# Kernel optimization log

Hardware: AMD Instinct MI355X
Metric: run time of the kernel (lower is better)

The kernel has to match this reference:

```python
import jax, jax.numpy as jnp
import numpy as np

ENT = 500000
REL = 1000
D = 128
N = 65536


def setup_inputs() -> dict:
    key = jax.random.key(0)
    ks = jax.random.split(key, 9)
    pos_h = jax.random.randint(ks[0], (N,), 0, ENT)
    pos_t = jax.random.randint(ks[1], (N,), 0, ENT)
    pos_r = jax.random.randint(ks[2], (N,), 0, REL)
    neg_h = jax.random.randint(ks[3], (N,), 0, ENT)
    neg_t = jax.random.randint(ks[4], (N,), 0, ENT)
    neg_r = jax.random.randint(ks[5], (N,), 0, REL)
    # entity embeddings: xavier-init then L2-row-normalized
    ent = jax.random.normal(ks[6], (ENT, D), dtype=jnp.float32)
    ent = ent / jnp.linalg.norm(ent, axis=1, keepdims=True)
    # vvrel embeddings: plain randn (sized entity_total in the original)
    vvrel = jax.random.normal(ks[7], (ENT, D), dtype=jnp.float32)
    # relation bases: L2-row-normalized
    bases = jax.random.normal(ks[8], (REL, D), dtype=jnp.float32)
    bases = bases / jnp.linalg.norm(bases, axis=1, keepdims=True)
    return {"pos_h": pos_h, "pos_t": pos_t, "pos_r": pos_r,
            "neg_h": neg_h, "neg_t": neg_t, "neg_r": neg_r,
            "ent_emb": ent, "vvrel_emb": vvrel, "bases": bases}


def _hyperplane_project(x, v):
    # (I - v v^T / (v.v)) x, applied row-wise without materializing [N,d,d]
    coef = jnp.sum(v * x, axis=-1, keepdims=True) / jnp.sum(v * v, axis=-1, keepdims=True)
    return x - coef * v


def reference(pos_h, pos_t, pos_r, neg_h, neg_t, neg_r, ent_emb, vvrel_emb, bases):
    v_pos = bases[pos_r]  # [N, D]; original uses pos_r projection for BOTH pos and neg
    ph = _hyperplane_project(ent_emb[pos_h], v_pos)
    pt = _hyperplane_project(ent_emb[pos_t], v_pos)
    pr = _hyperplane_project(vvrel_emb[pos_r], v_pos)
    nh = _hyperplane_project(ent_emb[neg_h], v_pos)
    nt = _hyperplane_project(ent_emb[neg_t], v_pos)
    nr = _hyperplane_project(vvrel_emb[neg_r], v_pos)
    # L1_flag = True
    pos = jnp.sum(jnp.abs(ph + pr - pt), axis=1)
    neg = jnp.sum(jnp.abs(nh + nr - nt), axis=1)
    return (pos, neg)
```

## Files before the change

### kernel.cpp

```cpp
#include <hip/hip_runtime.h>

#define NSAMP 65536
#define DDIM  128

__global__ __launch_bounds__(256) void transh_kernel(
    const int* __restrict__ pos_h, const int* __restrict__ pos_t, const int* __restrict__ pos_r,
    const int* __restrict__ neg_h, const int* __restrict__ neg_t, const int* __restrict__ neg_r,
    const float* __restrict__ ent, const float* __restrict__ vvrel, const float* __restrict__ bases,
    float* __restrict__ out)
{
    const int tid  = blockIdx.x * blockDim.x + threadIdx.x;
    const int samp = tid >> 5;
    const int sub  = threadIdx.x & 31;
    if (samp >= NSAMP) return;

    const int ph_i = pos_h[samp];
    const int pt_i = pos_t[samp];
    const int pr_i = pos_r[samp];
    const int nh_i = neg_h[samp];
    const int nt_i = neg_t[samp];
    const int nr_i = neg_r[samp];

    const float4* v4   = (const float4*)(bases + (size_t)pr_i * DDIM);
    const float4* ph4  = (const float4*)(ent   + (size_t)ph_i * DDIM);
    const float4* pt4  = (const float4*)(ent   + (size_t)pt_i * DDIM);
    const float4* prv4 = (const float4*)(vvrel + (size_t)pr_i * DDIM);
    const float4* nh4  = (const float4*)(ent   + (size_t)nh_i * DDIM);
    const float4* nt4  = (const float4*)(ent   + (size_t)nt_i * DDIM);
    const float4* nrv4 = (const float4*)(vvrel + (size_t)nr_i * DDIM);

    const float4 v  = v4[sub];
    const float4 a  = ph4[sub];
    const float4 c  = pt4[sub];
    const float4 b  = prv4[sub];
    const float4 na = nh4[sub];
    const float4 nc = nt4[sub];
    const float4 nb = nrv4[sub];

    float4 sp, sn;
    sp.x = a.x + b.x - c.x;  sp.y = a.y + b.y - c.y;
    sp.z = a.z + b.z - c.z;  sp.w = a.w + b.w - c.w;
    sn.x = na.x + nb.x - nc.x;  sn.y = na.y + nb.y - nc.y;
    sn.z = na.z + nb.z - nc.z;  sn.w = na.w + nb.w - nc.w;

    float vv  = v.x * v.x + v.y * v.y + v.z * v.z + v.w * v.w;
    float vsp = v.x * sp.x + v.y * sp.y + v.z * sp.z + v.w * sp.w;
    float vsn = v.x * sn.x + v.y * sn.y + v.z * sn.z + v.w * sn.w;

    #pragma unroll
    for (int off = 16; off > 0; off >>= 1) {
        vv  += __shfl_xor(vv,  off, 64);
        vsp += __shfl_xor(vsp, off, 64);
        vsn += __shfl_xor(vsn, off, 64);
    }

    const float cp = vsp / vv;
    const float cn = vsn / vv;

    float ap = fabsf(sp.x - cp * v.x) + fabsf(sp.y - cp * v.y)
             + fabsf(sp.z - cp * v.z) + fabsf(sp.w - cp * v.w);
    float an = fabsf(sn.x - cn * v.x) + fabsf(sn.y - cn * v.y)
             + fabsf(sn.z - cn * v.z) + fabsf(sn.w - cn * v.w);

    #pragma unroll
    for (int off = 16; off > 0; off >>= 1) {
        ap += __shfl_xor(ap, off, 64);
        an += __shfl_xor(an, off, 64);
    }

    if (sub == 0) {
        out[samp]         = ap;
        out[NSAMP + samp] = an;
    }
}

extern "C" void kernel_launch(void* const* d_in, const int* in_sizes, int n_in,
                              void* d_out, int out_size, void* d_ws, size_t ws_size,
                              hipStream_t stream) {
    const int*   pos_h = (const int*)d_in[0];
    const int*   pos_t = (const int*)d_in[1];
    const int*   pos_r = (const int*)d_in[2];
    const int*   neg_h = (const int*)d_in[3];
    const int*   neg_t = (const int*)d_in[4];
    const int*   neg_r = (const int*)d_in[5];
    const float* ent   = (const float*)d_in[6];
    const float* vvrel = (const float*)d_in[7];
    const float* bases = (const float*)d_in[8];
    float* out = (float*)d_out;

    const int threads = 256;
    const int blocks  = (NSAMP * 32) / threads;
    transh_kernel<<<blocks, threads, 0, stream>>>(
        pos_h, pos_t, pos_r, neg_h, neg_t, neg_r, ent, vvrel, bases, out);
}
```

Baseline: 419.4 us.

## Process four samples per half-wave with double-buffered row gathers

Each 32-lane group now handles four consecutive samples instead of one. All indices are loaded up front, and the seven gathered embedding rows for the next sample are prefetched into a second register buffer while the current sample is reduced. The goal is to keep more gather loads in flight per wave and to hide memory latency behind the shuffle reductions. In exchange the grid is four times smaller and register use rises, which may lower occupancy. The bounds check was also dropped, which is safe only because NSAMP divides evenly.

```diff
diff --git a/kernel.cpp b/kernel.cpp
--- a/kernel.cpp
+++ b/kernel.cpp
@@ -2,6 +2,7 @@
 
 #define NSAMP 65536
 #define DDIM  128
+#define SPT   4
 
 __global__ __launch_bounds__(256) void transh_kernel(
     const int* __restrict__ pos_h, const int* __restrict__ pos_t, const int* __restrict__ pos_r,
@@ -10,67 +11,84 @@
     float* __restrict__ out)
 {
     const int tid  = blockIdx.x * blockDim.x + threadIdx.x;
-    const int samp = tid >> 5;
+    const int hw   = tid >> 5;
     const int sub  = threadIdx.x & 31;
-    if (samp >= NSAMP) return;
+    const int base = hw * SPT;
 
-    const int ph_i = pos_h[samp];
-    const int pt_i = pos_t[samp];
-    const int pr_i = pos_r[samp];
-    const int nh_i = neg_h[samp];
-    const int nt_i = neg_t[samp];
-    const int nr_i = neg_r[samp];
+    int iph[SPT], ipt[SPT], ipr[SPT], inh[SPT], itn[SPT], inr[SPT];
+    #pragma unroll
+    for (int k = 0; k < SPT; ++k) {
+        const int s = base + k;
+        iph[k] = pos_h[s];  ipt[k] = pos_t[s];  ipr[k] = pos_r[s];
+        inh[k] = neg_h[s];  itn[k] = neg_t[s];  inr[k] = neg_r[s];
+    }
 
-    const float4* v4   = (const float4*)(bases + (size_t)pr_i * DDIM);
-    const float4* ph4  = (const float4*)(ent   + (size_t)ph_i * DDIM);
-    const float4* pt4  = (const float4*)(ent   + (size_t)pt_i * DDIM);
-    const float4* prv4 = (const float4*)(vvrel + (size_t)pr_i * DDIM);
-    const float4* nh4  = (const float4*)(ent   + (size_t)nh_i * DDIM);
-    const float4* nt4  = (const float4*)(ent   + (size_t)nt_i * DDIM);
-    const float4* nrv4 = (const float4*)(vvrel + (size_t)nr_i * DDIM);
+    float4 V[2], A[2], B[2], C[2], NA[2], NB[2], NC[2];
 
-    const float4 v  = v4[sub];
-    const float4 a  = ph4[sub];
-    const float4 c  = pt4[sub];
-    const float4 b  = prv4[sub];
-    const float4 na = nh4[sub];
-    const float4 nc = nt4[sub];
-    const float4 nb = nrv4[sub];
-
-    float4 sp, sn;
-    sp.x = a.x + b.x - c.x;  sp.y = a.y + b.y - c.y;
-    sp.z = a.z + b.z - c.z;  sp.w = a.w + b.w - c.w;
-    sn.x = na.x + nb.x - nc.x;  sn.y = na.y + nb.y - nc.y;
-    sn.z = na.z + nb.z - nc.z;  sn.w = na.w + nb.w - nc.w;
-
-    float vv  = v.x * v.x + v.y * v.y + v.z * v.z + v.w * v.w;
-    float vsp = v.x * sp.x + v.y * sp.y + v.z * sp.z + v.w * sp.w;
-    float vsn = v.x * sn.x + v.y * sn.y + v.z * sn.z + v.w * sn.w;
+    {
+        V[0]  = ((const float4*)(bases + (size_t)ipr[0] * DDIM))[sub];
+        A[0]  = ((const float4*)(ent   + (size_t)iph[0] * DDIM))[sub];
+        C[0]  = ((const float4*)(ent   + (size_t)ipt[0] * DDIM))[sub];
+        B[0]  = ((const float4*)(vvrel + (size_t)ipr[0] * DDIM))[sub];
+        NA[0] = ((const float4*)(ent   + (size_t)inh[0] * DDIM))[sub];
+        NC[0] = ((const float4*)(ent   + (size_t)itn[0] * DDIM))[sub];
+        NB[0] = ((const float4*)(vvrel + (size_t)inr[0] * DDIM))[sub];
+    }
 
     #pragma unroll
-    for (int off = 16; off > 0; off >>= 1) {
-        vv  += __shfl_xor(vv,  off, 64);
-        vsp += __shfl_xor(vsp, off, 64);
-        vsn += __shfl_xor(vsn, off, 64);
-    }
+    for (int k = 0; k < SPT; ++k) {
+        const int cur = k & 1;
+        const int nxt = cur ^ 1;
+        if (k + 1 < SPT) {
+            V[nxt]  = ((const float4*)(bases + (size_t)ipr[k+1] * DDIM))[sub];
+            A[nxt]  = ((const float4*)(ent   + (size_t)iph[k+1] * DDIM))[sub];
+            C[nxt]  = ((const float4*)(ent   + (size_t)ipt[k+1] * DDIM))[sub];
+            B[nxt]  = ((const float4*)(vvrel + (size_t)ipr[k+1] * DDIM))[sub];
+            NA[nxt] = ((const float4*)(ent   + (size_t)inh[k+1] * DDIM))[sub];
+            NC[nxt] = ((const float4*)(ent   + (size_t)itn[k+1] * DDIM))[sub];
+            NB[nxt] = ((const float4*)(vvrel + (size_t)inr[k+1] * DDIM))[sub];
+        }
 
-    const float cp = vsp / vv;
-    const float cn = vsn / vv;
+        const float4 v  = V[cur];
+        const float4 a  = A[cur],  c  = C[cur],  b  = B[cur];
+        const float4 na = NA[cur], nc = NC[cur], nb = NB[cur];
 
-    float ap = fabsf(sp.x - cp * v.x) + fabsf(sp.y - cp * v.y)
-             + fabsf(sp.z - cp * v.z) + fabsf(sp.w - cp * v.w);
-    float an = fabsf(sn.x - cn * v.x) + fabsf(sn.y - cn * v.y)
-             + fabsf(sn.z - cn * v.z) + fabsf(sn.w - cn * v.w);
+        float4 sp, sn;
+        sp.x = a.x + b.x - c.x;   sp.y = a.y + b.y - c.y;
+        sp.z = a.z + b.z - c.z;   sp.w = a.w + b.w - c.w;
+        sn.x = na.x + nb.x - nc.x; sn.y = na.y + nb.y - nc.y;
+        sn.z = na.z + nb.z - nc.z; sn.w = na.w + nb.w - nc.w;
 
-    #pragma unroll
-    for (int off = 16; off > 0; off >>= 1) {
-        ap += __shfl_xor(ap, off, 64);
-        an += __shfl_xor(an, off, 64);
-    }
+        float vv  = v.x * v.x  + v.y * v.y  + v.z * v.z  + v.w * v.w;
+        float vsp = v.x * sp.x + v.y * sp.y + v.z * sp.z + v.w * sp.w;
+        float vsn = v.x * sn.x + v.y * sn.y + v.z * sn.z + v.w * sn.w;
 
-    if (sub == 0) {
-        out[samp]         = ap;
-        out[NSAMP + samp] = an;
+        #pragma unroll
+        for (int off = 16; off > 0; off >>= 1) {
+            vv  += __shfl_xor(vv,  off, 64);
+            vsp += __shfl_xor(vsp, off, 64);
+            vsn += __shfl_xor(vsn, off, 64);
+        }
+
+        const float cp = vsp / vv;
+        const float cn = vsn / vv;
+
+        float ap = fabsf(sp.x - cp * v.x) + fabsf(sp.y - cp * v.y)
+                 + fabsf(sp.z - cp * v.z) + fabsf(sp.w - cp * v.w);
+        float an = fabsf(sn.x - cn * v.x) + fabsf(sn.y - cn * v.y)
+                 + fabsf(sn.z - cn * v.z) + fabsf(sn.w - cn * v.w);
+
+        #pragma unroll
+        for (int off = 16; off > 0; off >>= 1) {
+            ap += __shfl_xor(ap, off, 64);
+            an += __shfl_xor(an, off, 64);
+        }
+
+        if (sub == 0) {
+            const int s = base + k;
+            out[s]         = ap;
+            out[NSAMP + s] = an;
+        }
     }
 }
 
@@ -89,7 +107,7 @@
     float* out = (float*)d_out;
 
     const int threads = 256;
-    const int blocks  = (NSAMP * 32) / threads;
+    const int blocks  = (NSAMP / SPT) * 32 / threads;
     transh_kernel<<<blocks, threads, 0, stream>>>(
         pos_h, pos_t, pos_r, neg_h, neg_t, neg_r, ent, vvrel, bases, out);
 }
```

Measured after the change: 422.3 us. No clear change (+0.7%).
